# Optimization experiments

Measured on AMD Instinct MI355X. Metric: run time of the kernel, lower is better.

Reference implementation:

```python
import jax, jax.numpy as jnp
import numpy as np

N = 100000   # nodes
E = 3200000  # edges (avg degree 32)
G = 512      # graphs in batch
IN = 128     # in_channels
H1, C1 = 8, 8  # conv1 heads, per-head channels
OUT = 64     # out_channels (conv2, 1 head)
NEG_SLOPE = 0.2


def setup_inputs() -> dict:
    key = jax.random.key(0)
    ks = jax.random.split(key, 12)
    s = 0.1
    return dict(
        x=jax.random.normal(ks[0], (N, IN), jnp.float32),
        edge_index=jax.random.randint(ks[1], (2, E), 0, N),
        batch=jnp.sort(jax.random.randint(ks[2], (N,), 0, G)),
        W1=jax.random.normal(ks[3], (IN, H1 * C1), jnp.float32) * s,
        att_src1=jax.random.normal(ks[4], (H1, C1), jnp.float32) * s,
        att_dst1=jax.random.normal(ks[5], (H1, C1), jnp.float32) * s,
        b1=jnp.zeros((H1 * C1,), jnp.float32),
        W2=jax.random.normal(ks[6], (H1 * C1, OUT), jnp.float32) * s,
        att_src2=jax.random.normal(ks[7], (1, OUT), jnp.float32) * s,
        att_dst2=jax.random.normal(ks[8], (1, OUT), jnp.float32) * s,
        b2=jnp.zeros((OUT,), jnp.float32),
        lw1=jax.random.normal(ks[9], (OUT, 128), jnp.float32) * s,
        lb1=jnp.zeros((128,), jnp.float32),
        lw2=jax.random.normal(ks[10], (128, 1), jnp.float32) * s,
        lb2=jnp.zeros((1,), jnp.float32),
    )


def gat_layer(x, src, dst, W, a_src, a_dst, bias, heads, outc):
    # PyG GATConv (eval mode): linear -> per-edge leaky_relu attention ->
    # segment softmax over incoming edges per dst -> weighted scatter-add.
    n = x.shape[0]
    h = (x @ W).reshape(n, heads, outc)                      # [N,H,C]
    a_s = jnp.einsum('nhc,hc->nh', h, a_src)                 # [N,H]
    a_d = jnp.einsum('nhc,hc->nh', h, a_dst)
    e = jax.nn.leaky_relu(a_s[src] + a_d[dst], NEG_SLOPE)    # [E',H]
    m = jax.ops.segment_max(e, dst, num_segments=n)
    m = jax.lax.stop_gradient(jnp.where(jnp.isfinite(m), m, 0.0))
    ex = jnp.exp(e - m[dst])
    denom = jax.ops.segment_sum(ex, dst, num_segments=n)
    alpha = ex / jnp.maximum(denom[dst], 1e-16)              # [E',H]
    out = jax.ops.segment_sum(h[src] * alpha[:, :, None], dst, num_segments=n)
    return out.reshape(n, heads * outc) + bias


def reference(x, W1, att_src1, att_dst1, b1, W2, att_src2, att_dst2, b2,
              lw1, lb1, lw2, lb2, edge_index, batch):
    n = x.shape[0]
    loops = jnp.arange(n)                                    # add_self_loops=True
    src = jnp.concatenate([edge_index[0], loops])
    dst = jnp.concatenate([edge_index[1], loops])
    h = jax.nn.elu(gat_layer(x, src, dst, W1, att_src1, att_dst1, b1, H1, C1))
    h = gat_layer(h, src, dst, W2, att_src2, att_dst2, b2, 1, OUT)  # [N,OUT]
    # global_mean_pool
    s = jax.ops.segment_sum(h, batch, num_segments=G)
    cnt = jax.ops.segment_sum(jnp.ones((n, 1), h.dtype), batch, num_segments=G)
    g = s / jnp.maximum(cnt, 1.0)                            # [G,OUT]
    g = jax.nn.elu(g @ lw1 + lb1)
    return g @ lw2 + lb2                                     # [G,1]
```

## Files before the change

### kernel.cpp

```cpp
#include <hip/hip_runtime.h>
#include <hip/hip_fp16.h>
#include <math.h>

#define NN   100000
#define EE   3200000
#define GG   512
#define INC  128
#define D1   64
#define OUTC 64
#define HID  128
#define NEG  0.2f

#define BINS   782
#define BNODE  128
#define BSHIFT 7
#define BMASK  127
#define BCAP   4800
#define BKBLK 1563
#define NGB 391

typedef __attribute__((ext_vector_type(2))) float v2f;


__global__ __launch_bounds__(256, 3)
void k_fused(const int* __restrict__ srcv, const int* __restrict__ dstv,
             int* __restrict__ cursor, int* __restrict__ bucket,
             const float* __restrict__ x, const float* __restrict__ W1,
             const float* __restrict__ att_s, const float* __restrict__ att_d,
             unsigned int* __restrict__ rec, float* __restrict__ a_d) {
    __shared__ __align__(16) char smem[49152];
    int tid = threadIdx.x;
    if (blockIdx.x < NGB) {
        float4* sW4 = (float4*)smem;
        float (*sxT)[256] = (float(*)[256])(smem + 32768);
        const float4* W4 = (const float4*)W1;
        for (int i = tid; i < 128 * 16; i += 256) sW4[i] = W4[i];
        int node0 = blockIdx.x * 256;
        int rg = tid >> 3, cg = tid & 7;
        float acc[8][8];
#pragma unroll
        for (int ii = 0; ii < 8; ++ii)
#pragma unroll
            for (int jj = 0; jj < 8; ++jj) acc[ii][jj] = 0.f;
        const float4* x4 = (const float4*)x;
        for (int kt = 0; kt < 8; ++kt) {
            if (kt) __syncthreads();
#pragma unroll
            for (int q = 0; q < 4; ++q) {
                int i = q * 256 + tid;
                int r = i >> 2, kc = i & 3;
                int gn = node0 + r;
                float4 v = {0.f, 0.f, 0.f, 0.f};
                if (gn < NN) v = x4[(size_t)gn * 32 + kt * 4 + kc];
                int cs = r ^ (kc << 3);
                sxT[kc * 4 + 0][cs] = v.x;
                sxT[kc * 4 + 1][cs] = v.y;
                sxT[kc * 4 + 2][cs] = v.z;
                sxT[kc * 4 + 3][cs] = v.w;
            }
            __syncthreads();
#pragma unroll 4
            for (int kk = 0; kk < 16; ++kk) {
                int sw = (kk >> 2) << 3;
                const float* xr = &sxT[kk][(rg * 8) ^ sw];
                float4 xa = *(const float4*)xr;
                float4 xb = *(const float4*)(xr + 4);
                int kg = kt * 16 + kk;
                float4 wa = sW4[kg * 16 + cg * 2];
                float4 wb = sW4[kg * 16 + cg * 2 + 1];
                float xv[8] = {xa.x, xa.y, xa.z, xa.w, xb.x, xb.y, xb.z, xb.w};
                float wv[8] = {wa.x, wa.y, wa.z, wa.w, wb.x, wb.y, wb.z, wb.w};
#pragma unroll
                for (int ii = 0; ii < 8; ++ii)
#pragma unroll
                    for (int jj = 0; jj < 8; ++jj)
                        acc[ii][jj] = fmaf(xv[ii], wv[jj], acc[ii][jj]);
            }
        }
        float4 s0 = ((const float4*)att_s)[cg * 2];
        float4 s1 = ((const float4*)att_s)[cg * 2 + 1];
        float4 d0 = ((const float4*)att_d)[cg * 2];
        float4 d1 = ((const float4*)att_d)[cg * 2 + 1];
        uint2* hp2 = (uint2*)rec;
        __half* ash = (__half*)rec;
#pragma unroll
        for (int ii = 0; ii < 8; ++ii) {
            int n = node0 + rg * 8 + ii;
            if (n < NN) {
                float* a = acc[ii];
                int p0 = __builtin_amdgcn_cvt_pk_fp8_f32(a[0], a[1], 0, false);
                p0 = __builtin_amdgcn_cvt_pk_fp8_f32(a[2], a[3], p0, true);
                int p1 = __builtin_amdgcn_cvt_pk_fp8_f32(a[4], a[5], 0, false);
                p1 = __builtin_amdgcn_cvt_pk_fp8_f32(a[6], a[7], p1, true);
                uint2 pk; pk.x = (unsigned)p0; pk.y = (unsigned)p1;
                hp2[n * 16 + cg] = pk;
                float as = a[0] * s0.x;
                as = fmaf(a[1], s0.y, as); as = fmaf(a[2], s0.z, as);
                as = fmaf(a[3], s0.w, as); as = fmaf(a[4], s1.x, as);
                as = fmaf(a[5], s1.y, as); as = fmaf(a[6], s1.z, as);
                as = fmaf(a[7], s1.w, as);
                float ad = a[0] * d0.x;
                ad = fmaf(a[1], d0.y, ad); ad = fmaf(a[2], d0.z, ad);
                ad = fmaf(a[3], d0.w, ad); ad = fmaf(a[4], d1.x, ad);
                ad = fmaf(a[5], d1.y, ad); ad = fmaf(a[6], d1.z, ad);
                ad = fmaf(a[7], d1.w, ad);
                ash[n * 64 + 32 + cg] = __float2half(as);
                a_d[n * 8 + cg] = ad;
            }
        }
    } else {
        int* hcnt  = (int*)smem;
        int* hbase = hcnt + BINS;
        for (int i = tid; i < BINS; i += 256) hcnt[i] = 0;
        __syncthreads();
        int e0 = (blockIdx.x - NGB) * 2048;
        int bn[8], rk[8], pk[8];
#pragma unroll
        for (int q = 0; q < 8; ++q) {
            int e = e0 + q * 256 + tid;
            if (e < EE) {
                int s = srcv[e], d = dstv[e];
                bn[q] = d >> BSHIFT;
                pk[q] = (s << BSHIFT) | (d & BMASK);
                rk[q] = atomicAdd(&hcnt[bn[q]], 1);
            } else bn[q] = -1;
        }
        __syncthreads();
        for (int i = tid; i < BINS; i += 256) {
            int c = hcnt[i];
            hbase[i] = c ? atomicAdd(&cursor[i], c) : 0;
        }
        __syncthreads();
#pragma unroll
        for (int q = 0; q < 8; ++q) {
            if (bn[q] >= 0) {
                int p = hbase[bn[q]] + rk[q];
                if (p < BCAP) bucket[bn[q] * BCAP + p] = pk[q];
            }
        }
    }
}

__global__ __launch_bounds__(256)
void k_binCSR(const int* __restrict__ cursor, const int* __restrict__ bucket,
              int* __restrict__ col, int* __restrict__ rbeg, int* __restrict__ rend) {
    __shared__ int sseg[BCAP];
    __shared__ int cnt_[BNODE];
    __shared__ int tmp[BNODE];
    __shared__ int cur[BNODE];
    int b = blockIdx.x, tid = threadIdx.x;
    if (tid < BNODE) cnt_[tid] = 0;
    __syncthreads();
    int m = cursor[b]; if (m > BCAP) m = BCAP;
    const int* seg = bucket + b * BCAP;
    for (int i = tid; i < m; i += 256) {
        int v = seg[i];
        sseg[i] = v;
        atomicAdd(&cnt_[v & BMASK], 1);
    }
    __syncthreads();
    if (tid < BNODE) tmp[tid] = cnt_[tid];
    __syncthreads();
    for (int off = 1; off < BNODE; off <<= 1) {
        int t = (tid >= off && tid < BNODE) ? tmp[tid - off] : 0;
        __syncthreads();
        if (tid < BNODE) tmp[tid] += t;
        __syncthreads();
    }
    if (tid < BNODE) {
        int excl = tmp[tid] - cnt_[tid];
        int n = b * BNODE + tid;
        if (n < NN) {
            rbeg[n] = b * BCAP + excl;
            rend[n] = b * BCAP + excl + cnt_[tid];
        }
        cur[tid] = excl;
    }
    __syncthreads();
    for (int i = tid; i < m; i += 256) {
        int pkv = sseg[i];
        int r = atomicAdd(&cur[pkv & BMASK], 1);
        col[b * BCAP + r] = pkv >> BSHIFT;
    }
}

__global__ __launch_bounds__(256, 8)
void k_gat_agg1(const int* __restrict__ rbeg, const int* __restrict__ rend,
                const int* __restrict__ col,
                const unsigned int* __restrict__ rec, const float* __restrict__ a_d,
                const float* __restrict__ b1, float* __restrict__ out) {
    int wv = threadIdx.x >> 6;
    int lane = threadIdx.x & 63;
    int half = lane >> 5;
    int d = blockIdx.x * 8 + wv * 2 + half;
    int gs = (lane >> 3) & 3;
    int l = lane & 7;
    int rb = rbeg[d], re = rend[d];
    float adh = a_d[d * 8 + l];
    const uint2* hp = (const uint2*)rec;
    const __half* asr = (const __half*)rec;
    uint2 rself = hp[d * 16 + l];
    float asself = __half2float(asr[d * 64 + 32 + l]);
    float ac[8] = {0.f,0.f,0.f,0.f,0.f,0.f,0.f,0.f};
    float denom = 0.f;
    int e = rb + gs;
    int s[4];
#pragma unroll
    for (int q = 0; q < 4; ++q) s[q] = col[e + 4 * q];
    for (; e + 12 < re; ) {
        uint2 rr[4]; float asv[4]; int sn[4];
#pragma unroll
        for (int q = 0; q < 4; ++q) rr[q] = hp[(unsigned)(s[q] * 16 + l)];
#pragma unroll
        for (int q = 0; q < 4; ++q) asv[q] = __half2float(asr[(unsigned)(s[q] * 64 + 32 + l)]);
        int en = e + 16;
#pragma unroll
        for (int q = 0; q < 4; ++q) sn[q] = col[en + 4 * q];
#pragma unroll
        for (int q = 0; q < 4; ++q) {
            float xx = asv[q] + adh;
            xx = xx >= 0.f ? xx : NEG * xx;
            float w = __expf(xx);
            denom += w;
            v2f f0 = __builtin_amdgcn_cvt_pk_f32_fp8((int)rr[q].x, false);
            v2f f1 = __builtin_amdgcn_cvt_pk_f32_fp8((int)rr[q].x, true);
            v2f f2 = __builtin_amdgcn_cvt_pk_f32_fp8((int)rr[q].y, false);
            v2f f3 = __builtin_amdgcn_cvt_pk_f32_fp8((int)rr[q].y, true);
            ac[0] = fmaf(f0.x, w, ac[0]); ac[1] = fmaf(f0.y, w, ac[1]);
            ac[2] = fmaf(f1.x, w, ac[2]); ac[3] = fmaf(f1.y, w, ac[3]);
            ac[4] = fmaf(f2.x, w, ac[4]); ac[5] = fmaf(f2.y, w, ac[5]);
            ac[6] = fmaf(f3.x, w, ac[6]); ac[7] = fmaf(f3.y, w, ac[7]);
        }
        e = en;
#pragma unroll
        for (int q = 0; q < 4; ++q) s[q] = sn[q];
    }
    for (; e < re; e += 4) {
        int s0 = col[e];
        uint2 r0 = hp[(unsigned)(s0 * 16 + l)];
        float x0 = __half2float(asr[(unsigned)(s0 * 64 + 32 + l)]) + adh;
        x0 = x0 >= 0.f ? x0 : NEG * x0;
        float w0 = __expf(x0);
        denom += w0;
        v2f f0 = __builtin_amdgcn_cvt_pk_f32_fp8((int)r0.x, false);
        v2f f1 = __builtin_amdgcn_cvt_pk_f32_fp8((int)r0.x, true);
        v2f f2 = __builtin_amdgcn_cvt_pk_f32_fp8((int)r0.y, false);
        v2f f3 = __builtin_amdgcn_cvt_pk_f32_fp8((int)r0.y, true);
        ac[0] = fmaf(f0.x, w0, ac[0]); ac[1] = fmaf(f0.y, w0, ac[1]);
        ac[2] = fmaf(f1.x, w0, ac[2]); ac[3] = fmaf(f1.y, w0, ac[3]);
        ac[4] = fmaf(f2.x, w0, ac[4]); ac[5] = fmaf(f2.y, w0, ac[5]);
        ac[6] = fmaf(f3.x, w0, ac[6]); ac[7] = fmaf(f3.y, w0, ac[7]);
    }
    if (gs == 0) {
        float es = asself + adh;
        es = es >= 0.f ? es : NEG * es;
        float w = __expf(es);
        denom += w;
        v2f f0 = __builtin_amdgcn_cvt_pk_f32_fp8((int)rself.x, false);
        v2f f1 = __builtin_amdgcn_cvt_pk_f32_fp8((int)rself.x, true);
        v2f f2 = __builtin_amdgcn_cvt_pk_f32_fp8((int)rself.y, false);
        v2f f3 = __builtin_amdgcn_cvt_pk_f32_fp8((int)rself.y, true);
        ac[0] = fmaf(f0.x, w, ac[0]); ac[1] = fmaf(f0.y, w, ac[1]);
        ac[2] = fmaf(f1.x, w, ac[2]); ac[3] = fmaf(f1.y, w, ac[3]);
        ac[4] = fmaf(f2.x, w, ac[4]); ac[5] = fmaf(f2.y, w, ac[5]);
        ac[6] = fmaf(f3.x, w, ac[6]); ac[7] = fmaf(f3.y, w, ac[7]);
    }
#pragma unroll
    for (int i = 0; i < 8; ++i) {
        ac[i] += __shfl_xor(ac[i], 8, 64);
        ac[i] += __shfl_xor(ac[i], 16, 64);
    }
    denom += __shfl_xor(denom, 8, 64);
    denom += __shfl_xor(denom, 16, 64);
    if (gs == 0) {
        float inv = 1.0f / denom;
        float4 b0 = ((const float4*)b1)[l * 2];
        float4 b4 = ((const float4*)b1)[l * 2 + 1];
        float4 r0, r1;
        r0.x = fmaf(ac[0], inv, b0.x); r0.x = r0.x > 0.f ? r0.x : expm1f(r0.x);
        r0.y = fmaf(ac[1], inv, b0.y); r0.y = r0.y > 0.f ? r0.y : expm1f(r0.y);
        r0.z = fmaf(ac[2], inv, b0.z); r0.z = r0.z > 0.f ? r0.z : expm1f(r0.z);
        r0.w = fmaf(ac[3], inv, b0.w); r0.w = r0.w > 0.f ? r0.w : expm1f(r0.w);
        r1.x = fmaf(ac[4], inv, b4.x); r1.x = r1.x > 0.f ? r1.x : expm1f(r1.x);
        r1.y = fmaf(ac[5], inv, b4.y); r1.y = r1.y > 0.f ? r1.y : expm1f(r1.y);
        r1.z = fmaf(ac[6], inv, b4.z); r1.z = r1.z > 0.f ? r1.z : expm1f(r1.z);
        r1.w = fmaf(ac[7], inv, b4.w); r1.w = r1.w > 0.f ? r1.w : expm1f(r1.w);
        ((float4*)out)[d * 16 + l * 2]     = r0;
        ((float4*)out)[d * 16 + l * 2 + 1] = r1;
    }
}

__global__ __launch_bounds__(256, 3)
void k_lin2(const float* __restrict__ hin, const float* __restrict__ W2,
            const float* __restrict__ att_s, const float* __restrict__ att_d,
            unsigned int* __restrict__ rec, float* __restrict__ a_d) {
    __shared__ float4 sW4[D1 * 16];
    __shared__ float sxT[32][256];
    int tid = threadIdx.x;
    const float4* W4 = (const float4*)W2;
    for (int i = tid; i < D1 * 16; i += 256) sW4[i] = W4[i];
    int node0 = blockIdx.x * 256;
    int rg = tid >> 3, cg = tid & 7;
    float acc[8][8];
#pragma unroll
    for (int ii = 0; ii < 8; ++ii)
#pragma unroll
        for (int jj = 0; jj < 8; ++jj) acc[ii][jj] = 0.f;
    const float4* x4 = (const float4*)hin;
    for (int kt = 0; kt < 2; ++kt) {
        if (kt) __syncthreads();
#pragma unroll
        for (int q = 0; q < 8; ++q) {
            int i = q * 256 + tid;
            int r = i >> 3, kc = i & 7;
            int gn = node0 + r;
            float4 v = {0.f, 0.f, 0.f, 0.f};
            if (gn < NN) v = x4[(size_t)gn * 16 + kt * 8 + kc];
            int cs = r ^ (kc << 3);
            sxT[kc * 4 + 0][cs] = v.x;
            sxT[kc * 4 + 1][cs] = v.y;
            sxT[kc * 4 + 2][cs] = v.z;
            sxT[kc * 4 + 3][cs] = v.w;
        }
        __syncthreads();
#pragma unroll 4
        for (int kk = 0; kk < 32; ++kk) {
            int sw = (kk >> 2) << 3;
            const float* xr = &sxT[kk][(rg * 8) ^ sw];
            float4 xa = *(const float4*)xr;
            float4 xb = *(const float4*)(xr + 4);
            int kg = kt * 32 + kk;
            float4 wa = sW4[kg * 16 + cg * 2];
            float4 wb = sW4[kg * 16 + cg * 2 + 1];
            float xv[8] = {xa.x, xa.y, xa.z, xa.w, xb.x, xb.y, xb.z, xb.w};
            float wv[8] = {wa.x, wa.y, wa.z, wa.w, wb.x, wb.y, wb.z, wb.w};
#pragma unroll
            for (int ii = 0; ii < 8; ++ii)
#pragma unroll
                for (int jj = 0; jj < 8; ++jj)
                    acc[ii][jj] = fmaf(xv[ii], wv[jj], acc[ii][jj]);
        }
    }
    float4 s0 = ((const float4*)att_s)[cg * 2];
    float4 s1 = ((const float4*)att_s)[cg * 2 + 1];
    float4 d0 = ((const float4*)att_d)[cg * 2];
    float4 d1 = ((const float4*)att_d)[cg * 2 + 1];
    uint2* hp2 = (uint2*)rec;
#pragma unroll
    for (int ii = 0; ii < 8; ++ii) {
        int n = node0 + rg * 8 + ii;
        if (n < NN) {
            float* a = acc[ii];
            int p0 = __builtin_amdgcn_cvt_pk_fp8_f32(a[0], a[1], 0, false);
            p0 = __builtin_amdgcn_cvt_pk_fp8_f32(a[2], a[3], p0, true);
            int p1 = __builtin_amdgcn_cvt_pk_fp8_f32(a[4], a[5], 0, false);
            p1 = __builtin_amdgcn_cvt_pk_fp8_f32(a[6], a[7], p1, true);
            uint2 pk; pk.x = (unsigned)p0; pk.y = (unsigned)p1;
            hp2[n * 16 + cg] = pk;
            float vs = a[0] * s0.x;
            vs = fmaf(a[1], s0.y, vs); vs = fmaf(a[2], s0.z, vs);
            vs = fmaf(a[3], s0.w, vs); vs = fmaf(a[4], s1.x, vs);
            vs = fmaf(a[5], s1.y, vs); vs = fmaf(a[6], s1.z, vs);
            vs = fmaf(a[7], s1.w, vs);
            float vd = a[0] * d0.x;
            vd = fmaf(a[1], d0.y, vd); vd = fmaf(a[2], d0.z, vd);
            vd = fmaf(a[3], d0.w, vd); vd = fmaf(a[4], d1.x, vd);
            vd = fmaf(a[5], d1.y, vd); vd = fmaf(a[6], d1.z, vd);
            vd = fmaf(a[7], d1.w, vd);
            vs += __shfl_xor(vs, 1, 64); vs += __shfl_xor(vs, 2, 64);
            vs += __shfl_xor(vs, 4, 64);
            vd += __shfl_xor(vd, 1, 64); vd += __shfl_xor(vd, 2, 64);
            vd += __shfl_xor(vd, 4, 64);
            if (cg == 0) {
                ((float*)rec)[(size_t)n * 32 + 16] = vs;
                a_d[n] = vd;
            }
        }
    }
}

__global__ __launch_bounds__(256, 8)
void k_gat_agg2(const int* __restrict__ rbeg, const int* __restrict__ rend,
                const int* __restrict__ col,
                const unsigned int* __restrict__ rec, const float* __restrict__ a_d,
                const float* __restrict__ b2, const int* __restrict__ batch,
                float* __restrict__ pool, float* __restrict__ cnt) {
    __shared__ float sv[8][64];
    __shared__ int sgi[8];
    int wv = threadIdx.x >> 6;
    int lane = threadIdx.x & 63;
    int half = lane >> 5;
    int idx = wv * 2 + half;
    int d = blockIdx.x * 8 + idx;
    int gs = (lane >> 3) & 3;
    int l = lane & 7;
    int rb = rbeg[d], re = rend[d];
    float ad = a_d[d];
    const uint2* hp = (const uint2*)rec;
    const float* recf = (const float*)rec;
    uint2 rself = hp[d * 16 + l];
    float asself = recf[d * 32 + 16];
    if (gs == 0 && l == 0) sgi[idx] = batch[d];
    float ac[8] = {0.f,0.f,0.f,0.f,0.f,0.f,0.f,0.f};
    float denom = 0.f;
    int e = rb + gs;
    int s[4];
#pragma unroll
    for (int q = 0; q < 4; ++q) s[q] = col[e + 4 * q];
    for (; e + 12 < re; ) {
        uint2 rr[4]; float asv[4]; int sn[4];
#pragma unroll
        for (int q = 0; q < 4; ++q) rr[q] = hp[(unsigned)(s[q] * 16 + l)];
#pragma unroll
        for (int q = 0; q < 4; ++q) asv[q] = recf[(unsigned)(s[q] * 32 + 16)];
        int en = e + 16;
#pragma unroll
        for (int q = 0; q < 4; ++q) sn[q] = col[en + 4 * q];
#pragma unroll
        for (int q = 0; q < 4; ++q) {
            float xx = asv[q] + ad;
            xx = xx >= 0.f ? xx : NEG * xx;
            float w = __expf(xx);
            denom += w;
            v2f f0 = __builtin_amdgcn_cvt_pk_f32_fp8((int)rr[q].x, false);
            v2f f1 = __builtin_amdgcn_cvt_pk_f32_fp8((int)rr[q].x, true);
            v2f f2 = __builtin_amdgcn_cvt_pk_f32_fp8((int)rr[q].y, false);
            v2f f3 = __builtin_amdgcn_cvt_pk_f32_fp8((int)rr[q].y, true);
            ac[0] = fmaf(f0.x, w, ac[0]); ac[1] = fmaf(f0.y, w, ac[1]);
            ac[2] = fmaf(f1.x, w, ac[2]); ac[3] = fmaf(f1.y, w, ac[3]);
            ac[4] = fmaf(f2.x, w, ac[4]); ac[5] = fmaf(f2.y, w, ac[5]);
            ac[6] = fmaf(f3.x, w, ac[6]); ac[7] = fmaf(f3.y, w, ac[7]);
        }
        e = en;
#pragma unroll
        for (int q = 0; q < 4; ++q) s[q] = sn[q];
    }
    for (; e < re; e += 4) {
        int s0 = col[e];
        uint2 r0 = hp[(unsigned)(s0 * 16 + l)];
        float x0 = recf[(unsigned)(s0 * 32 + 16)] + ad;
        x0 = x0 >= 0.f ? x0 : NEG * x0;
        float w0 = __expf(x0);
        denom += w0;
        v2f f0 = __builtin_amdgcn_cvt_pk_f32_fp8((int)r0.x, false);
        v2f f1 = __builtin_amdgcn_cvt_pk_f32_fp8((int)r0.x, true);
        v2f f2 = __builtin_amdgcn_cvt_pk_f32_fp8((int)r0.y, false);
        v2f f3 = __builtin_amdgcn_cvt_pk_f32_fp8((int)r0.y, true);
        ac[0] = fmaf(f0.x, w0, ac[0]); ac[1] = fmaf(f0.y, w0, ac[1]);
        ac[2] = fmaf(f1.x, w0, ac[2]); ac[3] = fmaf(f1.y, w0, ac[3]);
        ac[4] = fmaf(f2.x, w0, ac[4]); ac[5] = fmaf(f2.y, w0, ac[5]);
        ac[6] = fmaf(f3.x, w0, ac[6]); ac[7] = fmaf(f3.y, w0, ac[7]);
    }
    if (gs == 0) {
        float es = asself + ad;
        es = es >= 0.f ? es : NEG * es;
        float w = __expf(es);
        denom += w;
        v2f f0 = __builtin_amdgcn_cvt_pk_f32_fp8((int)rself.x, false);
        v2f f1 = __builtin_amdgcn_cvt_pk_f32_fp8((int)rself.x, true);
        v2f f2 = __builtin_amdgcn_cvt_pk_f32_fp8((int)rself.y, false);
        v2f f3 = __builtin_amdgcn_cvt_pk_f32_fp8((int)rself.y, true);
        ac[0] = fmaf(f0.x, w, ac[0]); ac[1] = fmaf(f0.y, w, ac[1]);
        ac[2] = fmaf(f1.x, w, ac[2]); ac[3] = fmaf(f1.y, w, ac[3]);
        ac[4] = fmaf(f2.x, w, ac[4]); ac[5] = fmaf(f2.y, w, ac[5]);
        ac[6] = fmaf(f3.x, w, ac[6]); ac[7] = fmaf(f3.y, w, ac[7]);
    }
#pragma unroll
    for (int i = 0; i < 8; ++i) {
        ac[i] += __shfl_xor(ac[i], 8, 64);
        ac[i] += __shfl_xor(ac[i], 16, 64);
    }
    denom += __shfl_xor(denom, 8, 64);
    denom += __shfl_xor(denom, 16, 64);
    if (gs == 0) {
        float inv = 1.0f / denom;
#pragma unroll
        for (int i = 0; i < 8; ++i)
            sv[idx][l * 8 + i] = fmaf(ac[i], inv, b2[l * 8 + i]);
    }
    __syncthreads();
    int tid = threadIdx.x;
    if (tid < 64) {
        float acc = sv[0][tid]; int curg = sgi[0];
        for (int r = 1; r < 8; ++r) {
            if (sgi[r] == curg) acc += sv[r][tid];
            else { atomicAdd(&pool[curg * 64 + tid], acc); curg = sgi[r]; acc = sv[r][tid]; }
        }
        atomicAdd(&pool[curg * 64 + tid], acc);
    } else if (tid == 64) {
        float c = 1.f; int curg = sgi[0];
        for (int r = 1; r < 8; ++r) {
            if (sgi[r] == curg) c += 1.f;
            else { atomicAdd(&cnt[curg], c); curg = sgi[r]; c = 1.f; }
        }
        atomicAdd(&cnt[curg], c);
    }
}

__global__ __launch_bounds__(128)
void k_mlp(const float* __restrict__ pool, const float* __restrict__ cnt,
           const float* __restrict__ lw1, const float* __restrict__ lb1,
           const float* __restrict__ lw2, const float* __restrict__ lb2,
           float* __restrict__ out) {
    __shared__ float sg[OUTC];
    __shared__ float sh[HID];
    int g = blockIdx.x, tid = threadIdx.x;
    float c = fmaxf(cnt[g], 1.0f);
    if (tid < OUTC) sg[tid] = pool[g * OUTC + tid] / c;
    __syncthreads();
    float acc = lb1[tid];
#pragma unroll 8
    for (int k = 0; k < OUTC; ++k)
        acc = fmaf(sg[k], lw1[k * HID + tid], acc);
    acc = acc > 0.f ? acc : expm1f(acc);
    sh[tid] = acc * lw2[tid];
    __syncthreads();
    for (int off = 64; off >= 1; off >>= 1) {
        if (tid < off) sh[tid] += sh[tid + off];
        __syncthreads();
    }
    if (tid == 0) out[g] = sh[0] + lb2[0];
}

extern "C" void kernel_launch(void* const* d_in, const int* in_sizes, int n_in,
                              void* d_out, int out_size, void* d_ws, size_t ws_size,
                              hipStream_t stream) {
    const float* x    = (const float*)d_in[0];
    const int*   ei   = (const int*)d_in[1];
    const int*   batch= (const int*)d_in[2];
    const float* W1   = (const float*)d_in[3];
    const float* as1  = (const float*)d_in[4];
    const float* ad1  = (const float*)d_in[5];
    const float* b1   = (const float*)d_in[6];
    const float* W2   = (const float*)d_in[7];
    const float* as2  = (const float*)d_in[8];
    const float* ad2  = (const float*)d_in[9];
    const float* b2   = (const float*)d_in[10];
    const float* lw1  = (const float*)d_in[11];
    const float* lb1  = (const float*)d_in[12];
    const float* lw2  = (const float*)d_in[13];
    const float* lb2  = (const float*)d_in[14];
    float* out = (float*)d_out;

    unsigned int* REC = (unsigned int*)d_ws;
    float* B    = (float*)(REC + (size_t)NN * 32);
    float* aD1  = B + (size_t)NN * 64;
    float* aD2  = aD1 + (size_t)NN * 8;
    float* pool = aD2 + NN;
    float* cntp = pool + GG * 64;
    int* rbeg   = (int*)(cntp + GG);
    int* rend   = rbeg + NN;
    int* cursor = rend + NN;
    int* bucket = cursor + BINS;
    int* colv   = bucket + (size_t)BINS * BCAP;

    const int* srcv = ei;
    const int* dstv = ei + EE;

    hipMemsetAsync(cursor, 0, BINS * sizeof(int), stream);
    hipMemsetAsync(pool, 0, (size_t)(GG * 64 + GG) * sizeof(float), stream);

    k_fused<<<NGB + BKBLK, 256, 0, stream>>>(srcv, dstv, cursor, bucket,
                                             x, W1, as1, ad1, REC, aD1);
    k_binCSR<<<BINS, 256, 0, stream>>>(cursor, bucket, colv, rbeg, rend);

    k_gat_agg1<<<NN / 8, 256, 0, stream>>>(rbeg, rend, colv, REC, aD1, b1, B);

    k_lin2    <<<NGB, 256, 0, stream>>>(B, W2, as2, ad2, REC, aD2);
    k_gat_agg2<<<NN / 8, 256, 0, stream>>>(rbeg, rend, colv, REC, aD2, b2, batch, pool, cntp);

    k_mlp<<<GG, 128, 0, stream>>>(pool, cntp, lw1, lb1, lw2, lb2, out);
}
```

Measured before the change: 352.1 us.

## Fuse layer-2 linear transform and attention scores into layer-1 aggregation epilogue

Removes the separate k_lin2 kernel by having each k_gat_agg1 block stage its 8 aggregated rows in shared memory, multiply them by a transposed W2 held in LDS, and write fp8-packed features plus the src/dst attention scalars directly. This drops the fp32 intermediate B (N×64) write and re-read and one kernel launch. A second record buffer REC2 is added so that layer 2 no longer overwrites REC while other blocks of agg1 are still gathering from it. In exchange every agg1 block reloads W2 into LDS and uses more shared memory plus a block barrier, which may lower occupancy for the gather-bound kernel.

```diff
diff --git a/kernel.cpp b/kernel.cpp
--- a/kernel.cpp
+++ b/kernel.cpp
@@ -188,11 +188,26 @@
 void k_gat_agg1(const int* __restrict__ rbeg, const int* __restrict__ rend,
                 const int* __restrict__ col,
                 const unsigned int* __restrict__ rec, const float* __restrict__ a_d,
-                const float* __restrict__ b1, float* __restrict__ out) {
-    int wv = threadIdx.x >> 6;
-    int lane = threadIdx.x & 63;
+                const float* __restrict__ b1,
+                const float* __restrict__ W2, const float* __restrict__ att_s2,
+                const float* __restrict__ att_d2,
+                unsigned int* __restrict__ rec2, float* __restrict__ a_d2) {
+    __shared__ float sW2T[64][68];
+    __shared__ float4 sB4[8][16];
+    int tid = threadIdx.x;
+    for (int i = tid; i < 64 * 16; i += 256) {
+        float4 v = ((const float4*)W2)[i];
+        int k = i >> 4, jg = i & 15;
+        sW2T[jg * 4 + 0][k] = v.x;
+        sW2T[jg * 4 + 1][k] = v.y;
+        sW2T[jg * 4 + 2][k] = v.z;
+        sW2T[jg * 4 + 3][k] = v.w;
+    }
+    int wv = tid >> 6;
+    int lane = tid & 63;
     int half = lane >> 5;
-    int d = blockIdx.x * 8 + wv * 2 + half;
+    int idx = wv * 2 + half;
+    int d = blockIdx.x * 8 + idx;
     int gs = (lane >> 3) & 3;
     int l = lane & 7;
     int rb = rbeg[d], re = rend[d];
@@ -285,97 +300,43 @@
         r1.y = fmaf(ac[5], inv, b4.y); r1.y = r1.y > 0.f ? r1.y : expm1f(r1.y);
         r1.z = fmaf(ac[6], inv, b4.z); r1.z = r1.z > 0.f ? r1.z : expm1f(r1.z);
         r1.w = fmaf(ac[7], inv, b4.w); r1.w = r1.w > 0.f ? r1.w : expm1f(r1.w);
-        ((float4*)out)[d * 16 + l * 2]     = r0;
-        ((float4*)out)[d * 16 + l * 2 + 1] = r1;
-    }
-}
-
-__global__ __launch_bounds__(256, 3)
-void k_lin2(const float* __restrict__ hin, const float* __restrict__ W2,
-            const float* __restrict__ att_s, const float* __restrict__ att_d,
-            unsigned int* __restrict__ rec, float* __restrict__ a_d) {
-    __shared__ float4 sW4[D1 * 16];
-    __shared__ float sxT[32][256];
-    int tid = threadIdx.x;
-    const float4* W4 = (const float4*)W2;
-    for (int i = tid; i < D1 * 16; i += 256) sW4[i] = W4[i];
-    int node0 = blockIdx.x * 256;
-    int rg = tid >> 3, cg = tid & 7;
-    float acc[8][8];
-#pragma unroll
-    for (int ii = 0; ii < 8; ++ii)
-#pragma unroll
-        for (int jj = 0; jj < 8; ++jj) acc[ii][jj] = 0.f;
-    const float4* x4 = (const float4*)hin;
-    for (int kt = 0; kt < 2; ++kt) {
-        if (kt) __syncthreads();
-#pragma unroll
-        for (int q = 0; q < 8; ++q) {
-            int i = q * 256 + tid;
-            int r = i >> 3, kc = i & 7;
-            int gn = node0 + r;
-            float4 v = {0.f, 0.f, 0.f, 0.f};
-            if (gn < NN) v = x4[(size_t)gn * 16 + kt * 8 + kc];
-            int cs = r ^ (kc << 3);
-            sxT[kc * 4 + 0][cs] = v.x;
-            sxT[kc * 4 + 1][cs] = v.y;
-            sxT[kc * 4 + 2][cs] = v.z;
-            sxT[kc * 4 + 3][cs] = v.w;
-        }
-        __syncthreads();
-#pragma unroll 4
-        for (int kk = 0; kk < 32; ++kk) {
-            int sw = (kk >> 2) << 3;
-            const float* xr = &sxT[kk][(rg * 8) ^ sw];
-            float4 xa = *(const float4*)xr;
-            float4 xb = *(const float4*)(xr + 4);
-            int kg = kt * 32 + kk;
-            float4 wa = sW4[kg * 16 + cg * 2];
-            float4 wb = sW4[kg * 16 + cg * 2 + 1];
-            float xv[8] = {xa.x, xa.y, xa.z, xa.w, xb.x, xb.y, xb.z, xb.w};
-            float wv[8] = {wa.x, wa.y, wa.z, wa.w, wb.x, wb.y, wb.z, wb.w};
-#pragma unroll
-            for (int ii = 0; ii < 8; ++ii)
-#pragma unroll
-                for (int jj = 0; jj < 8; ++jj)
-                    acc[ii][jj] = fmaf(xv[ii], wv[jj], acc[ii][jj]);
-        }
-    }
-    float4 s0 = ((const float4*)att_s)[cg * 2];
-    float4 s1 = ((const float4*)att_s)[cg * 2 + 1];
-    float4 d0 = ((const float4*)att_d)[cg * 2];
-    float4 d1 = ((const float4*)att_d)[cg * 2 + 1];
-    uint2* hp2 = (uint2*)rec;
-#pragma unroll
-    for (int ii = 0; ii < 8; ++ii) {
-        int n = node0 + rg * 8 + ii;
-        if (n < NN) {
-            float* a = acc[ii];
-            int p0 = __builtin_amdgcn_cvt_pk_fp8_f32(a[0], a[1], 0, false);
-            p0 = __builtin_amdgcn_cvt_pk_fp8_f32(a[2], a[3], p0, true);
-            int p1 = __builtin_amdgcn_cvt_pk_fp8_f32(a[4], a[5], 0, false);
-            p1 = __builtin_amdgcn_cvt_pk_fp8_f32(a[6], a[7], p1, true);
-            uint2 pk; pk.x = (unsigned)p0; pk.y = (unsigned)p1;
-            hp2[n * 16 + cg] = pk;
-            float vs = a[0] * s0.x;
-            vs = fmaf(a[1], s0.y, vs); vs = fmaf(a[2], s0.z, vs);
-            vs = fmaf(a[3], s0.w, vs); vs = fmaf(a[4], s1.x, vs);
-            vs = fmaf(a[5], s1.y, vs); vs = fmaf(a[6], s1.z, vs);
-            vs = fmaf(a[7], s1.w, vs);
-            float vd = a[0] * d0.x;
-            vd = fmaf(a[1], d0.y, vd); vd = fmaf(a[2], d0.z, vd);
-            vd = fmaf(a[3], d0.w, vd); vd = fmaf(a[4], d1.x, vd);
-            vd = fmaf(a[5], d1.y, vd); vd = fmaf(a[6], d1.z, vd);
-            vd = fmaf(a[7], d1.w, vd);
-            vs += __shfl_xor(vs, 1, 64); vs += __shfl_xor(vs, 2, 64);
-            vs += __shfl_xor(vs, 4, 64);
-            vd += __shfl_xor(vd, 1, 64); vd += __shfl_xor(vd, 2, 64);
-            vd += __shfl_xor(vd, 4, 64);
-            if (cg == 0) {
-                ((float*)rec)[(size_t)n * 32 + 16] = vs;
-                a_d[n] = vd;
-            }
-        }
+        sB4[idx][l * 2]     = r0;
+        sB4[idx][l * 2 + 1] = r1;
+    }
+    __syncthreads();
+    int g2 = tid >> 5;
+    int t  = tid & 31;
+    int n2 = blockIdx.x * 8 + g2;
+    int j0 = t * 2, j1 = t * 2 + 1;
+    float h0 = 0.f, h1 = 0.f;
+#pragma unroll
+    for (int kq = 0; kq < 16; ++kq) {
+        float4 bv = sB4[g2][kq];
+        float4 w0 = *(const float4*)&sW2T[j0][kq * 4];
+        float4 w1 = *(const float4*)&sW2T[j1][kq * 4];
+        h0 = fmaf(bv.x, w0.x, h0); h0 = fmaf(bv.y, w0.y, h0);
+        h0 = fmaf(bv.z, w0.z, h0); h0 = fmaf(bv.w, w0.w, h0);
+        h1 = fmaf(bv.x, w1.x, h1); h1 = fmaf(bv.y, w1.y, h1);
+        h1 = fmaf(bv.z, w1.z, h1); h1 = fmaf(bv.w, w1.w, h1);
+    }
+    float vs = h0 * att_s2[j0];  vs = fmaf(h1, att_s2[j1], vs);
+    float vd = h0 * att_d2[j0];  vd = fmaf(h1, att_d2[j1], vd);
+#pragma unroll
+    for (int off = 1; off <= 16; off <<= 1) {
+        vs += __shfl_xor(vs, off, 64);
+        vd += __shfl_xor(vd, off, 64);
+    }
+    int pk16 = __builtin_amdgcn_cvt_pk_fp8_f32(h0, h1, 0, false);
+    int hi16 = __shfl(pk16, lane + 1, 64);
+    unsigned word = ((unsigned)pk16 & 0xFFFFu) | ((unsigned)hi16 << 16);
+    unsigned wy = (unsigned)__shfl((int)word, lane + 2, 64);
+    if ((t & 3) == 0) {
+        uint2 val; val.x = word; val.y = wy;
+        ((uint2*)rec2)[n2 * 16 + (t >> 2)] = val;
+    }
+    if (t == 0) {
+        ((float*)rec2)[(size_t)n2 * 32 + 16] = vs;
+        a_d2[n2] = vd;
     }
 }
 
@@ -542,9 +503,9 @@
     const float* lb2  = (const float*)d_in[14];
     float* out = (float*)d_out;
 
-    unsigned int* REC = (unsigned int*)d_ws;
-    float* B    = (float*)(REC + (size_t)NN * 32);
-    float* aD1  = B + (size_t)NN * 64;
+    unsigned int* REC  = (unsigned int*)d_ws;
+    unsigned int* REC2 = REC + (size_t)NN * 32;
+    float* aD1  = (float*)(REC2 + (size_t)NN * 32);
     float* aD2  = aD1 + (size_t)NN * 8;
     float* pool = aD2 + NN;
     float* cntp = pool + GG * 64;
@@ -564,10 +525,10 @@
                                              x, W1, as1, ad1, REC, aD1);
     k_binCSR<<<BINS, 256, 0, stream>>>(cursor, bucket, colv, rbeg, rend);
 
-    k_gat_agg1<<<NN / 8, 256, 0, stream>>>(rbeg, rend, colv, REC, aD1, b1, B);
-
-    k_lin2    <<<NGB, 256, 0, stream>>>(B, W2, as2, ad2, REC, aD2);
-    k_gat_agg2<<<NN / 8, 256, 0, stream>>>(rbeg, rend, colv, REC, aD2, b2, batch, pool, cntp);
+    k_gat_agg1<<<NN / 8, 256, 0, stream>>>(rbeg, rend, colv, REC, aD1, b1,
+                                           W2, as2, ad2, REC2, aD2);
+
+    k_gat_agg2<<<NN / 8, 256, 0, stream>>>(rbeg, rend, colv, REC2, aD2, b2, batch, pool, cntp);
 
     k_mlp<<<GG, 128, 0, stream>>>(pool, cntp, lw1, lb1, lw2, lb2, out);
 }
```

After: 354.3 us. No clear change (+0.6%).
